# Performance work log

Hardware: AMD Instinct MI355X
Metric: run time of the kernel (lower is better)

The kernel has to match this reference:

```python
import jax, jax.numpy as jnp
import numpy as np

INPUT_SIZE = 1024
HIDDEN_SIZE = 1024
BATCH = 8192


def setup_inputs() -> dict:
    key = jax.random.key(0)
    ks = jax.random.split(key, 10)
    s_in = 1.0 / np.sqrt(INPUT_SIZE)
    s_h = 1.0 / np.sqrt(HIDDEN_SIZE)
    return {
        "input": jax.random.normal(ks[0], (BATCH, INPUT_SIZE), jnp.float32),
        "hx": jax.random.normal(ks[1], (BATCH, HIDDEN_SIZE), jnp.float32),
        # weights stored [in, out] (transpose of torch Linear)
        "W_ih": jax.random.uniform(ks[2], (INPUT_SIZE, 2 * HIDDEN_SIZE), jnp.float32, -s_in, s_in),
        "b_ih": jax.random.uniform(ks[3], (2 * HIDDEN_SIZE,), jnp.float32, -s_in, s_in),
        "W_hh": jax.random.uniform(ks[4], (HIDDEN_SIZE, 2 * HIDDEN_SIZE), jnp.float32, -s_h, s_h),
        "b_hh": jax.random.uniform(ks[5], (2 * HIDDEN_SIZE,), jnp.float32, -s_h, s_h),
        "W_c": jax.random.uniform(ks[6], (INPUT_SIZE, HIDDEN_SIZE), jnp.float32, -s_in, s_in),
        "b_c": jax.random.uniform(ks[7], (HIDDEN_SIZE,), jnp.float32, -s_in, s_in),
        "W_hc": jax.random.uniform(ks[8], (HIDDEN_SIZE, HIDDEN_SIZE), jnp.float32, -s_h, s_h),
        "b_hc": jax.random.uniform(ks[9], (HIDDEN_SIZE,), jnp.float32, -s_h, s_h),
    }


def reference(input, hx, W_ih, b_ih, W_hh, b_hh, W_c, b_c, W_hc, b_hc):
    H = hx.shape[1]
    gates = jax.nn.sigmoid(input @ W_ih + b_ih + hx @ W_hh + b_hh)  # [B, 2H]
    z_t, r_t = gates[:, :H], gates[:, H:]
    candidate = jnp.tanh(input @ W_c + b_c + r_t * (hx @ W_hc + b_hc))
    return (1.0 - z_t) * hx + z_t * candidate
```

## Files before the change

### kernel.cpp

```cpp
#include <hip/hip_runtime.h>
#include <hip/hip_bf16.h>
#include <cmath>


typedef __attribute__((ext_vector_type(8))) short bf16x8;
typedef __attribute__((ext_vector_type(4))) float f32x4;
typedef unsigned int u32;

typedef const __attribute__((address_space(1))) u32 gu32;
typedef __attribute__((address_space(3))) u32 su32;

__device__ __forceinline__ unsigned short f2bf(float f) {
  union { float f; u32 u; } v; v.f = f;
  u32 u = v.u;
  u += 0x7FFFu + ((u >> 16) & 1u);
  return (unsigned short)(u >> 16);
}
__device__ __forceinline__ float bfu(u32 w) {
  union { u32 u; float f; } c; c.u = (w & 0xffffu) << 16; return c.f;
}
__device__ __forceinline__ void gload16(void* ldsp, const void* gp) {
  __builtin_amdgcn_global_load_lds((gu32*)gp, (su32*)ldsp, 16, 0, 0);
}
__device__ __forceinline__ float sigmf(float x) { return 1.0f / (1.0f + __expf(-x)); }

__global__ __launch_bounds__(256) void cvt2(
    const float* __restrict__ In, const float* __restrict__ Hx,
    const float* __restrict__ Wih, const float* __restrict__ Whh,
    const float* __restrict__ Wc,  const float* __restrict__ Whc,
    unsigned short* __restrict__ wsIn, unsigned short* __restrict__ wsHx,
    unsigned short* __restrict__ wsW)
{
  int bid = blockIdx.x;
  if (bid < 8192) {
    int gid = bid * 256 + threadIdx.x;
    const float* src; unsigned short* dst; int idx;
    if (gid < (1 << 20)) { src = In; dst = wsIn; idx = gid; }
    else                 { src = Hx; dst = wsHx; idx = gid - (1 << 20); }
    int m = idx >> 7, u = idx & 127;
    int kt = u >> 3, s = u & 7;
    const float4* p = (const float4*)(src + (size_t)m * 1024 + kt * 64 + s * 8);
    float4 a = p[0], b = p[1];
    int row = m & 255, mt = m >> 8;
    int sp = s ^ (row & 7);
    bf16x8 v;
    v[0] = (short)f2bf(a.x); v[1] = (short)f2bf(a.y); v[2] = (short)f2bf(a.z); v[3] = (short)f2bf(a.w);
    v[4] = (short)f2bf(b.x); v[5] = (short)f2bf(b.y); v[6] = (short)f2bf(b.z); v[7] = (short)f2bf(b.w);
    *(bf16x8*)(dst + (size_t)(mt * 16 + kt) * 16384 + row * 64 + sp * 8) = v;
  } else {
    int w = bid - 8192;
    int j = w / 384, rem = w % 384;
    int t = rem >> 3, s = rem & 7;
    int jj = j & 3, f = j >> 2;
    int row = threadIdx.x;
    const float* W; int NW, k0, ncol;
    if (t < 16)      { W = Wih; NW = 2048; k0 = t * 64 + s * 8;        ncol = f * 1024 + jj * 256 + row; }
    else if (t < 32) { W = Whh; NW = 2048; k0 = (t - 16) * 64 + s * 8; ncol = f * 1024 + jj * 256 + row; }
    else             { W = f ? Whc : Wc; NW = 1024; k0 = (t - 32) * 64 + s * 8; ncol = jj * 256 + row; }
    bf16x8 v;
    #pragma unroll
    for (int b = 0; b < 8; ++b) v[b] = (short)f2bf(W[(size_t)(k0 + b) * NW + ncol]);
    int sp = s ^ (row & 7);
    *(bf16x8*)(wsW + (size_t)(j * 48 + t) * 16384 + row * 64 + sp * 8) = v;
  }
}

__global__ __launch_bounds__(512, 2) void gru_gemm1(
    const unsigned short* __restrict__ wsIn, const unsigned short* __restrict__ wsHx,
    const unsigned short* __restrict__ wsW,
    unsigned short* __restrict__ actZ, unsigned short* __restrict__ actR,
    unsigned short* __restrict__ actC, unsigned short* __restrict__ actH,
    const float* __restrict__ bih, const float* __restrict__ bhh)
{
  __shared__ unsigned short lds[65536];
  char* LB = (char*)lds;
  const int tid = threadIdx.x, lane = tid & 63, wave = tid >> 6;
  const int wm = wave >> 2, wn = wave & 3;
  const int j = blockIdx.x & 7, i = blockIdx.x >> 3;
  const int jj = j & 3, f = j >> 2;
  const int r15 = lane & 15, q = lane >> 4, x7 = r15 & 7;

  int aOff[8][2], bOff[4][2];
  #pragma unroll
  for (int mr = 0; mr < 8; ++mr)
    #pragma unroll
    for (int kk = 0; kk < 2; ++kk)
      aOff[mr][kk] = (wm * 128 + mr * 16 + r15) * 128 + (((kk * 4 + q) ^ x7) << 4);
  #pragma unroll
  for (int nr = 0; nr < 4; ++nr)
    #pragma unroll
    for (int kk = 0; kk < 2; ++kk)
      bOff[nr][kk] = 65536 + (wn * 64 + nr * 16 + r15) * 128 + (((kk * 4 + q) ^ x7) << 4);

  const unsigned short* srcW  = wsW + (size_t)j * 48 * 16384;
  const unsigned short* srcA2 = f ? wsHx : wsIn;
  const int lo8 = lane * 8;

  auto aSrc = [&](int kt) -> const unsigned short* {
    const unsigned short* base; int t;
    if (kt < 16)      { base = wsIn;  t = kt; }
    else if (kt < 32) { base = wsHx;  t = kt - 16; }
    else              { base = srcA2; t = kt - 32; }
    return base + (size_t)(i * 16 + t) * 16384;
  };
  auto stageA = [&](int PB, int kt) {
    const unsigned short* s = aSrc(kt);
    #pragma unroll
    for (int c = 0; c < 4; ++c)
      gload16(LB + PB + (wave * 4 + c) * 1024, s + (wave * 4 + c) * 512 + lo8);
  };
  auto stageB = [&](int PB, int kt) {
    const unsigned short* s = srcW + (size_t)kt * 16384;
    #pragma unroll
    for (int c = 0; c < 4; ++c)
      gload16(LB + 65536 + PB + (wave * 4 + c) * 1024, s + (wave * 4 + c) * 512 + lo8);
  };

  f32x4 acc[8][4];
  #pragma unroll
  for (int mr = 0; mr < 8; ++mr)
    #pragma unroll
    for (int nr = 0; nr < 4; ++nr) acc[mr][nr] = (f32x4)(0.0f);

  #define MG(AF, BF, MRB, NRB)                                                      \
    __builtin_amdgcn_s_setprio(1);                                                  \
    _Pragma("unroll")                                                               \
    for (int mr_ = 0; mr_ < 4; ++mr_)                                               \
      _Pragma("unroll")                                                             \
      for (int nr_ = 0; nr_ < 2; ++nr_)                                             \
        _Pragma("unroll")                                                           \
        for (int kk_ = 0; kk_ < 2; ++kk_)                                           \
          acc[(MRB)+mr_][(NRB)+nr_] = __builtin_amdgcn_mfma_f32_16x16x32_bf16(      \
              AF[mr_][kk_], BF[nr_][kk_], acc[(MRB)+mr_][(NRB)+nr_], 0, 0, 0);      \
    __builtin_amdgcn_s_setprio(0);

  #define TILE(PB, KT, KTN)                                                         \
  {                                                                                 \
    bf16x8 a0[4][2], a1[4][2], b0[2][2], b1[2][2];                                  \
    _Pragma("unroll")                                                               \
    for (int mr_ = 0; mr_ < 4; ++mr_)                                               \
      _Pragma("unroll")                                                             \
      for (int kk_ = 0; kk_ < 2; ++kk_)                                             \
        a0[mr_][kk_] = *(const bf16x8*)(LB + (PB) + aOff[mr_][kk_]);                \
    _Pragma("unroll")                                                               \
    for (int nr_ = 0; nr_ < 2; ++nr_)                                               \
      _Pragma("unroll")                                                             \
      for (int kk_ = 0; kk_ < 2; ++kk_)                                             \
        b0[nr_][kk_] = *(const bf16x8*)(LB + (PB) + bOff[nr_][kk_]);                \
    MG(a0, b0, 0, 0)                                                                \
    _Pragma("unroll")                                                               \
    for (int nr_ = 0; nr_ < 2; ++nr_)                                               \
      _Pragma("unroll")                                                             \
      for (int kk_ = 0; kk_ < 2; ++kk_)                                             \
        b1[nr_][kk_] = *(const bf16x8*)(LB + (PB) + bOff[nr_ + 2][kk_]);            \
    MG(a0, b1, 0, 2)                                                                \
    _Pragma("unroll")                                                               \
    for (int mr_ = 0; mr_ < 4; ++mr_)                                               \
      _Pragma("unroll")                                                             \
      for (int kk_ = 0; kk_ < 2; ++kk_)                                             \
        a1[mr_][kk_] = *(const bf16x8*)(LB + (PB) + aOff[mr_ + 4][kk_]);            \
    MG(a1, b0, 4, 0)                                                                \
    asm volatile("s_waitcnt lgkmcnt(0)" ::: "memory");                              \
    __builtin_amdgcn_sched_barrier(0);                                              \
    __builtin_amdgcn_s_barrier();                                                   \
    __builtin_amdgcn_sched_barrier(0);                                              \
    stageA(PB, KTN);                                                                \
    MG(a1, b1, 4, 2)                                                                \
    stageB(PB, KTN);                                                                \
    asm volatile("s_waitcnt vmcnt(8)" ::: "memory");                                \
    __builtin_amdgcn_sched_barrier(0);                                              \
    __builtin_amdgcn_s_barrier();                                                   \
    __builtin_amdgcn_sched_barrier(0);                                              \
  }

  auto dump = [&](unsigned short* dst, bool gate, float* bg) {
    #pragma unroll
    for (int mr = 0; mr < 8; ++mr)
      #pragma unroll
      for (int nr = 0; nr < 4; ++nr) {
        f32x4 t = acc[mr][nr];
        float e0, e1, e2, e3;
        if (gate) {
          e0 = sigmf(t[0] + bg[nr]); e1 = sigmf(t[1] + bg[nr]);
          e2 = sigmf(t[2] + bg[nr]); e3 = sigmf(t[3] + bg[nr]);
        } else { e0 = t[0]; e1 = t[1]; e2 = t[2]; e3 = t[3]; }
        u32 lo = (u32)f2bf(e0) | ((u32)f2bf(e1) << 16);
        u32 hi = (u32)f2bf(e2) | ((u32)f2bf(e3) << 16);
        size_t F = ((size_t)(((i * 2 + wm) * 8 + mr) * 64 + jj * 16 + wn * 4 + nr)) * 256 + lane * 4;
        uint2 uv; uv.x = lo; uv.y = hi;
        *(uint2*)(dst + F) = uv;
        acc[mr][nr] = (f32x4)(0.0f);
      }
  };

  stageA(0, 0);     stageB(0, 0);
  stageA(32768, 1); stageB(32768, 1);
  asm volatile("s_waitcnt vmcnt(0)" ::: "memory");
  __builtin_amdgcn_s_barrier();
  __builtin_amdgcn_sched_barrier(0);

  #pragma unroll 1
  for (int it = 0; it < 16; ++it) {
    int kt = 2 * it;
    TILE(0,     kt,     kt + 2)
    TILE(32768, kt + 1, kt + 3)
  }

  {
    float bg[4];
    #pragma unroll
    for (int nr = 0; nr < 4; ++nr) {
      int gn = jj * 256 + wn * 64 + nr * 16 + r15;
      int np = f ? 1024 + gn : gn;
      bg[nr] = bih[np] + bhh[np];
    }
    dump(f ? actR : actZ, true, bg);
  }

  #pragma unroll 1
  for (int it = 0; it < 8; ++it) {
    int kt = 32 + 2 * it;
    int n0 = kt + 2 <= 47 ? kt + 2 : 47;
    int n1 = kt + 3 <= 47 ? kt + 3 : 47;
    TILE(0,     kt,     n0)
    TILE(32768, kt + 1, n1)
  }

  dump(f ? actH : actC, false, nullptr);
  #undef TILE
  #undef MG
}

__global__ __launch_bounds__(256) void gru_final(
    const unsigned short* __restrict__ actZ, const unsigned short* __restrict__ actR,
    const unsigned short* __restrict__ actC, const unsigned short* __restrict__ actH,
    const float* __restrict__ Hx, const float* __restrict__ bc,
    const float* __restrict__ bhc, float* __restrict__ out)
{
  int T = blockIdx.x * 256 + threadIdx.x;
  int lane = T & 63, fr = T >> 6;
  int nr = fr & 3, wn = (fr >> 2) & 3, jj = (fr >> 4) & 3, mr = (fr >> 6) & 7, wmI = fr >> 9;
  int n  = jj * 256 + wn * 64 + nr * 16 + (lane & 15);
  int m0 = wmI * 128 + mr * 16 + ((lane >> 4) << 2);
  size_t off = (size_t)T * 4;
  uint2 zq = *(const uint2*)(actZ + off);
  uint2 rq = *(const uint2*)(actR + off);
  uint2 cq = *(const uint2*)(actC + off);
  uint2 hq = *(const uint2*)(actH + off);
  float bcv = bc[n], bhv = bhc[n];
  u32 zw[2] = { zq.x, zq.y }, rw[2] = { rq.x, rq.y };
  u32 cw[2] = { cq.x, cq.y }, hw[2] = { hq.x, hq.y };
  #pragma unroll
  for (int v = 0; v < 4; ++v) {
    int sh = (v & 1) * 16, ix = v >> 1;
    float z = bfu(zw[ix] >> sh);
    float r = bfu(rw[ix] >> sh);
    float c = bfu(cw[ix] >> sh);
    float h = bfu(hw[ix] >> sh);
    size_t adr = (size_t)(m0 + v) * 1024 + n;
    float hx = Hx[adr];
    float cand = tanhf(c + bcv + r * (h + bhv));
    out[adr] = (1.0f - z) * hx + z * cand;
  }
}

__global__ __launch_bounds__(256) void cvt_m(
    const float* __restrict__ In, const float* __restrict__ Hx,
    const float* __restrict__ Wih, const float* __restrict__ Whh,
    const float* __restrict__ Wc,  const float* __restrict__ Whc,
    unsigned short* __restrict__ wsIn, unsigned short* __restrict__ wsHx,
    unsigned short* __restrict__ wsWih, unsigned short* __restrict__ wsWhh,
    unsigned short* __restrict__ wsWc,  unsigned short* __restrict__ wsWhc)
{
  int bid = blockIdx.x;
  if (bid < 8192) {
    int gid = bid * 256 + threadIdx.x;
    const float* src; unsigned short* dst; int idx;
    if (gid < (1 << 20)) { src = In; dst = wsIn; idx = gid; }
    else                 { src = Hx; dst = wsHx; idx = gid - (1 << 20); }
    int m = idx >> 7, t = idx & 127;
    const float4* s = (const float4*)(src + (size_t)m * 1024 + t * 8);
    float4 a = s[0], b = s[1];
    int row = m & 127;
    size_t tile = (size_t)(m >> 7) * 32 + (t >> 2);
    int sw = (t & 3) ^ ((row >> 1) & 3);
    bf16x8 v;
    v[0] = (short)f2bf(a.x); v[1] = (short)f2bf(a.y); v[2] = (short)f2bf(a.z); v[3] = (short)f2bf(a.w);
    v[4] = (short)f2bf(b.x); v[5] = (short)f2bf(b.y); v[6] = (short)f2bf(b.z); v[7] = (short)f2bf(b.w);
    *(bf16x8*)(dst + tile * 4096 + row * 32 + sw * 8) = v;
  } else {
    int wb = bid - 8192;
    const float* W; unsigned short* dst; int NW; int local;
    if (wb < 1024)      { W = Wih; dst = wsWih; NW = 2048; local = wb; }
    else if (wb < 2048) { W = Whh; dst = wsWhh; NW = 2048; local = wb - 1024; }
    else if (wb < 2560) { W = Wc;  dst = wsWc;  NW = 1024; local = wb - 2048; }
    else                { W = Whc; dst = wsWhc; NW = 1024; local = wb - 2560; }
    int nb = local >> 5, kb = local & 31;
    int n  = nb * 64 + (threadIdx.x & 63);
    int k0 = kb * 32 + (threadIdx.x >> 6) * 8;
    bf16x8 v;
    #pragma unroll
    for (int b = 0; b < 8; ++b) v[b] = (short)f2bf(W[(size_t)(k0 + b) * NW + n]);
    int row = n & 63;
    size_t tile = (size_t)(n >> 6) * 32 + (k0 >> 5);
    int sw = ((k0 >> 3) & 3) ^ ((row >> 1) & 3);
    *(bf16x8*)(dst + tile * 2048 + row * 32 + sw * 8) = v;
  }
}

__global__ __launch_bounds__(256, 2) void gemm_m(
    const unsigned short* __restrict__ wsIn, const unsigned short* __restrict__ wsHx,
    const unsigned short* __restrict__ wsWih, const unsigned short* __restrict__ wsWhh,
    const unsigned short* __restrict__ wsWc, const unsigned short* __restrict__ wsWhc,
    const float* __restrict__ Hx,
    const float* __restrict__ bih, const float* __restrict__ bhh,
    const float* __restrict__ bc, const float* __restrict__ bhc,
    float* __restrict__ out)
{
  __shared__ unsigned short lds[20480];
  const int tid  = threadIdx.x;
  const int lane = tid & 63;
  const int wave = tid >> 6;
  const int wm = wave >> 1, wn = wave & 1;
  const int bid = blockIdx.x;
  const int j = bid & 15;
  const int i = bid >> 4;
  const unsigned short* srcB[10];
  int strd[10];
  #pragma unroll
  for (int c0 = 0; c0 < 10; ++c0) {
    int c = wave * 10 + c0;
    const unsigned short* p; int st;
    if (c < 8)       { p = wsIn + (size_t)i * 131072 + c * 512;        st = 4096; }
    else if (c < 16) { p = wsHx + (size_t)i * 131072 + (c - 8) * 512;  st = 4096; }
    else {
      int t = (c - 16) >> 2, cc = (c - 16) & 3;
      const unsigned short* base; int nb;
      if (t == 0)      { base = wsWih; nb = j; }
      else if (t == 1) { base = wsWih; nb = j + 16; }
      else if (t == 2) { base = wsWhh; nb = j; }
      else if (t == 3) { base = wsWhh; nb = j + 16; }
      else if (t == 4) { base = wsWc;  nb = j; }
      else             { base = wsWhc; nb = j; }
      p = base + (size_t)nb * 65536 + cc * 512;
      st = 2048;
    }
    srcB[c0] = p + lane * 8;
    strd[c0] = st;
  }
  f32x4 accZ[4][2], accR[4][2], accC[4][2], accH[4][2];
  #pragma unroll
  for (int a = 0; a < 4; ++a)
    #pragma unroll
    for (int b = 0; b < 2; ++b) {
      accZ[a][b] = (f32x4)(0.0f); accR[a][b] = (f32x4)(0.0f);
      accC[a][b] = (f32x4)(0.0f); accH[a][b] = (f32x4)(0.0f);
    }
  const int r15 = lane & 15;
  const int q   = lane >> 4;
  int aOff[4], wOff[2];
  #pragma unroll
  for (int mr = 0; mr < 4; ++mr) {
    int row = wm * 64 + mr * 16 + r15;
    aOff[mr] = row * 32 + ((q ^ ((row >> 1) & 3)) << 3);
  }
  #pragma unroll
  for (int nr = 0; nr < 2; ++nr) {
    int row = wn * 32 + nr * 16 + r15;
    wOff[nr] = row * 32 + ((q ^ ((row >> 1) & 3)) << 3);
  }
  for (int s = 0; s < 32; ++s) {
    __syncthreads();
    #pragma unroll
    for (int c0 = 0; c0 < 10; ++c0)
      gload16((void*)&lds[(wave * 10 + c0) * 512],
              (const void*)(srcB[c0] + (size_t)s * strd[c0]));
    __syncthreads();
    bf16x8 aIn[4], aHx[4];
    #pragma unroll
    for (int mr = 0; mr < 4; ++mr) {
      aIn[mr] = *(const bf16x8*)&lds[aOff[mr]];
      aHx[mr] = *(const bf16x8*)&lds[4096 + aOff[mr]];
    }
    bf16x8 wf[6][2];
    #pragma unroll
    for (int t = 0; t < 6; ++t)
      #pragma unroll
      for (int nr = 0; nr < 2; ++nr)
        wf[t][nr] = *(const bf16x8*)&lds[8192 + t * 2048 + wOff[nr]];
    #pragma unroll
    for (int mr = 0; mr < 4; ++mr)
      #pragma unroll
      for (int nr = 0; nr < 2; ++nr) {
        accZ[mr][nr] = __builtin_amdgcn_mfma_f32_16x16x32_bf16(aIn[mr], wf[0][nr], accZ[mr][nr], 0, 0, 0);
        accZ[mr][nr] = __builtin_amdgcn_mfma_f32_16x16x32_bf16(aHx[mr], wf[2][nr], accZ[mr][nr], 0, 0, 0);
        accR[mr][nr] = __builtin_amdgcn_mfma_f32_16x16x32_bf16(aIn[mr], wf[1][nr], accR[mr][nr], 0, 0, 0);
        accR[mr][nr] = __builtin_amdgcn_mfma_f32_16x16x32_bf16(aHx[mr], wf[3][nr], accR[mr][nr], 0, 0, 0);
        accC[mr][nr] = __builtin_amdgcn_mfma_f32_16x16x32_bf16(aIn[mr], wf[4][nr], accC[mr][nr], 0, 0, 0);
        accH[mr][nr] = __builtin_amdgcn_mfma_f32_16x16x32_bf16(aHx[mr], wf[5][nr], accH[mr][nr], 0, 0, 0);
      }
  }
  const int n0 = j * 64 + wn * 32;
  const int m0 = i * 128 + wm * 64;
  #pragma unroll
  for (int nr = 0; nr < 2; ++nr) {
    int n = n0 + nr * 16 + r15;
    float bz  = bih[n] + bhh[n];
    float br  = bih[1024 + n] + bhh[1024 + n];
    float bcv = bc[n], bhcv = bhc[n];
    #pragma unroll
    for (int mr = 0; mr < 4; ++mr) {
      #pragma unroll
      for (int v = 0; v < 4; ++v) {
        int m = m0 + mr * 16 + q * 4 + v;
        float z  = sigmf(accZ[mr][nr][v] + bz);
        float rr = sigmf(accR[mr][nr][v] + br);
        float cd = tanhf(accC[mr][nr][v] + bcv + rr * (accH[mr][nr][v] + bhcv));
        float h  = Hx[(size_t)m * 1024 + n];
        out[(size_t)m * 1024 + n] = (1.0f - z) * h + z * cd;
      }
    }
  }
}

__global__ __launch_bounds__(256) void gru_fallback(
    const float* __restrict__ In, const float* __restrict__ Hx,
    const float* __restrict__ Wih, const float* __restrict__ bih,
    const float* __restrict__ Whh, const float* __restrict__ bhh,
    const float* __restrict__ Wc, const float* __restrict__ bc,
    const float* __restrict__ Whc, const float* __restrict__ bhc,
    float* __restrict__ out)
{
  __shared__ float sIn[64][17], sHx[64][17];
  __shared__ float sW[6][16][68];
  const int tid = threadIdx.x;
  const int j = blockIdx.x & 15, i = blockIdx.x >> 4;
  const int tx = tid & 15, ty = tid >> 4;
  float accZ[4][4] = {}, accR[4][4] = {}, accC[4][4] = {}, accH[4][4] = {};
  const int ms = tid >> 2, kq = (tid & 3) * 4;
  const int wk = tid >> 4, wn4 = (tid & 15) * 4;
  for (int k0 = 0; k0 < 1024; k0 += 16) {
    __syncthreads();
    {
      float4 a = *(const float4*)&In[(size_t)(i * 64 + ms) * 1024 + k0 + kq];
      sIn[ms][kq] = a.x; sIn[ms][kq + 1] = a.y; sIn[ms][kq + 2] = a.z; sIn[ms][kq + 3] = a.w;
      float4 b = *(const float4*)&Hx[(size_t)(i * 64 + ms) * 1024 + k0 + kq];
      sHx[ms][kq] = b.x; sHx[ms][kq + 1] = b.y; sHx[ms][kq + 2] = b.z; sHx[ms][kq + 3] = b.w;
    }
    {
      float4 w0 = *(const float4*)&Wih[(size_t)(k0 + wk) * 2048 + j * 64 + wn4];
      float4 w1 = *(const float4*)&Wih[(size_t)(k0 + wk) * 2048 + 1024 + j * 64 + wn4];
      float4 w2 = *(const float4*)&Whh[(size_t)(k0 + wk) * 2048 + j * 64 + wn4];
      float4 w3 = *(const float4*)&Whh[(size_t)(k0 + wk) * 2048 + 1024 + j * 64 + wn4];
      float4 w4 = *(const float4*)&Wc[(size_t)(k0 + wk) * 1024 + j * 64 + wn4];
      float4 w5 = *(const float4*)&Whc[(size_t)(k0 + wk) * 1024 + j * 64 + wn4];
      sW[0][wk][wn4] = w0.x; sW[0][wk][wn4+1] = w0.y; sW[0][wk][wn4+2] = w0.z; sW[0][wk][wn4+3] = w0.w;
      sW[1][wk][wn4] = w1.x; sW[1][wk][wn4+1] = w1.y; sW[1][wk][wn4+2] = w1.z; sW[1][wk][wn4+3] = w1.w;
      sW[2][wk][wn4] = w2.x; sW[2][wk][wn4+1] = w2.y; sW[2][wk][wn4+2] = w2.z; sW[2][wk][wn4+3] = w2.w;
      sW[3][wk][wn4] = w3.x; sW[3][wk][wn4+1] = w3.y; sW[3][wk][wn4+2] = w3.z; sW[3][wk][wn4+3] = w3.w;
      sW[4][wk][wn4] = w4.x; sW[4][wk][wn4+1] = w4.y; sW[4][wk][wn4+2] = w4.z; sW[4][wk][wn4+3] = w4.w;
      sW[5][wk][wn4] = w5.x; sW[5][wk][wn4+1] = w5.y; sW[5][wk][wn4+2] = w5.z; sW[5][wk][wn4+3] = w5.w;
    }
    __syncthreads();
    for (int kk = 0; kk < 16; ++kk) {
      float aI[4], aH[4];
      #pragma unroll
      for (int im = 0; im < 4; ++im) { aI[im] = sIn[ty * 4 + im][kk]; aH[im] = sHx[ty * 4 + im][kk]; }
      #pragma unroll
      for (int jn = 0; jn < 4; ++jn) {
        float w0 = sW[0][kk][tx * 4 + jn], w1 = sW[1][kk][tx * 4 + jn], w2 = sW[2][kk][tx * 4 + jn];
        float w3 = sW[3][kk][tx * 4 + jn], w4 = sW[4][kk][tx * 4 + jn], w5 = sW[5][kk][tx * 4 + jn];
        #pragma unroll
        for (int im = 0; im < 4; ++im) {
          accZ[im][jn] += aI[im] * w0 + aH[im] * w2;
          accR[im][jn] += aI[im] * w1 + aH[im] * w3;
          accC[im][jn] += aI[im] * w4;
          accH[im][jn] += aH[im] * w5;
        }
      }
    }
  }
  #pragma unroll
  for (int jn = 0; jn < 4; ++jn) {
    int n = j * 64 + tx * 4 + jn;
    float bz  = bih[n] + bhh[n];
    float br  = bih[1024 + n] + bhh[1024 + n];
    float bcv = bc[n], bhcv = bhc[n];
    #pragma unroll
    for (int im = 0; im < 4; ++im) {
      int m = i * 64 + ty * 4 + im;
      float z  = sigmf(accZ[im][jn] + bz);
      float rr = sigmf(accR[im][jn] + br);
      float cd = tanhf(accC[im][jn] + bcv + rr * (accH[im][jn] + bhcv));
      float h  = Hx[(size_t)m * 1024 + n];
      out[(size_t)m * 1024 + n] = (1.0f - z) * h + z * cd;
    }
  }
}

extern "C" void kernel_launch(void* const* d_in, const int* in_sizes, int n_in,
                              void* d_out, int out_size, void* d_ws, size_t ws_size,
                              hipStream_t stream) {
  const float* In  = (const float*)d_in[0];
  const float* Hx  = (const float*)d_in[1];
  const float* Wih = (const float*)d_in[2];
  const float* bih = (const float*)d_in[3];
  const float* Whh = (const float*)d_in[4];
  const float* bhh = (const float*)d_in[5];
  const float* Wc  = (const float*)d_in[6];
  const float* bc  = (const float*)d_in[7];
  const float* Whc = (const float*)d_in[8];
  const float* bhc = (const float*)d_in[9];
  float* out = (float*)d_out;

  const size_t WS_BIG = 113246208ull;
  const size_t WS_MID = 46137344ull;
  if (ws_size >= WS_BIG) {
    unsigned short* ws   = (unsigned short*)d_ws;
    unsigned short* wsIn = ws;
    unsigned short* wsHx = ws + 8388608;
    unsigned short* wsW  = ws + 16777216;
    unsigned short* actZ = ws + 23068672;
    unsigned short* actR = ws + 31457280;
    unsigned short* actC = ws + 39845888;
    unsigned short* actH = ws + 48234496;
    cvt2<<<11264, 256, 0, stream>>>(In, Hx, Wih, Whh, Wc, Whc, wsIn, wsHx, wsW);
    gru_gemm1<<<256, 512, 0, stream>>>(wsIn, wsHx, wsW, actZ, actR, actC, actH, bih, bhh);
    gru_final<<<8192, 256, 0, stream>>>(actZ, actR, actC, actH, Hx, bc, bhc, out);
  } else if (ws_size >= WS_MID) {
    unsigned short* ws    = (unsigned short*)d_ws;
    unsigned short* wsIn  = ws;
    unsigned short* wsHx  = ws + 8388608;
    unsigned short* wsWih = ws + 16777216;
    unsigned short* wsWhh = ws + 18874368;
    unsigned short* wsWc  = ws + 20971520;
    unsigned short* wsWhc = ws + 22020096;
    cvt_m<<<11264, 256, 0, stream>>>(In, Hx, Wih, Whh, Wc, Whc,
                                     wsIn, wsHx, wsWih, wsWhh, wsWc, wsWhc);
    gemm_m<<<1024, 256, 0, stream>>>(wsIn, wsHx, wsWih, wsWhh, wsWc, wsWhc,
                                     Hx, bih, bhh, bc, bhc, out);
  } else {
    gru_fallback<<<2048, 256, 0, stream>>>(In, Hx, Wih, bih, Whh, bhh, Wc, bc, Whc, bhc, out);
  }
}
```

Before: 156.3 us.

## Fuse GRU epilogue into cooperative GEMM kernel with grid sync

Replaces the separate gru_final kernel with a cooperative launch: f==0 blocks dump the input-side candidate pre-activation, all blocks grid-sync, and f==1 blocks compute the final GRU output directly from their hc accumulators. This removes one kernel launch and the write and read of the actH intermediate. The TILE pipeline is also restructured with extra s_barriers interleaved between MFMA groups and LDS staging, plus a relaxed prologue wait (vmcnt(8) instead of vmcnt(0)). In exchange, the added barriers and the grid-wide sync may stall waves, and half of the blocks sit idle during the epilogue.

```diff
diff --git a/kernel.cpp b/kernel.cpp
--- a/kernel.cpp
+++ b/kernel.cpp
@@ -1,6 +1,9 @@
 #include <hip/hip_runtime.h>
 #include <hip/hip_bf16.h>
+#include <hip/hip_cooperative_groups.h>
 #include <cmath>
+
+namespace cg = cooperative_groups;
 
 
 typedef __attribute__((ext_vector_type(8))) short bf16x8;
@@ -23,6 +26,11 @@
   __builtin_amdgcn_global_load_lds((gu32*)gp, (su32*)ldsp, 16, 0, 0);
 }
 __device__ __forceinline__ float sigmf(float x) { return 1.0f / (1.0f + __expf(-x)); }
+
+#define SB0   __builtin_amdgcn_sched_barrier(0)
+#define BARR  __builtin_amdgcn_s_barrier()
+#define LGKM0 asm volatile("s_waitcnt lgkmcnt(0)" ::: "memory")
+#define VMC8  asm volatile("s_waitcnt vmcnt(8)" ::: "memory")
 
 __global__ __launch_bounds__(256) void cvt2(
     const float* __restrict__ In, const float* __restrict__ Hx,
@@ -65,15 +73,19 @@
   }
 }
 
-__global__ __launch_bounds__(512, 2) void gru_gemm1(
+__global__ __launch_bounds__(512, 2) void gru_coop(
     const unsigned short* __restrict__ wsIn, const unsigned short* __restrict__ wsHx,
     const unsigned short* __restrict__ wsW,
-    unsigned short* __restrict__ actZ, unsigned short* __restrict__ actR,
-    unsigned short* __restrict__ actC, unsigned short* __restrict__ actH,
-    const float* __restrict__ bih, const float* __restrict__ bhh)
+    unsigned short* __restrict__ actZ, unsigned short* __restrict__ actC,
+    unsigned short* __restrict__ actR,
+    const float* __restrict__ Hx,
+    const float* __restrict__ bih, const float* __restrict__ bhh,
+    const float* __restrict__ bc, const float* __restrict__ bhc,
+    float* __restrict__ out)
 {
   __shared__ unsigned short lds[65536];
   char* LB = (char*)lds;
+  cg::grid_group grid = cg::this_grid();
   const int tid = threadIdx.x, lane = tid & 63, wave = tid >> 6;
   const int wm = wave >> 2, wn = wave & 3;
   const int j = blockIdx.x & 7, i = blockIdx.x >> 3;
@@ -134,9 +146,10 @@
               AF[mr_][kk_], BF[nr_][kk_], acc[(MRB)+mr_][(NRB)+nr_], 0, 0, 0);      \
     __builtin_amdgcn_s_setprio(0);
 
-  #define TILE(PB, KT, KTN)                                                         \
+  #define TILE(PB, KTN)                                                             \
   {                                                                                 \
     bf16x8 a0[4][2], a1[4][2], b0[2][2], b1[2][2];                                  \
+                                               \
     _Pragma("unroll")                                                               \
     for (int mr_ = 0; mr_ < 4; ++mr_)                                               \
       _Pragma("unroll")                                                             \
@@ -147,30 +160,35 @@
       _Pragma("unroll")                                                             \
       for (int kk_ = 0; kk_ < 2; ++kk_)                                             \
         b0[nr_][kk_] = *(const bf16x8*)(LB + (PB) + bOff[nr_][kk_]);                \
+    BARR;                                                                           \
     MG(a0, b0, 0, 0)                                                                \
+    BARR;                                                                           \
+                                  \
     _Pragma("unroll")                                                               \
     for (int nr_ = 0; nr_ < 2; ++nr_)                                               \
       _Pragma("unroll")                                                             \
       for (int kk_ = 0; kk_ < 2; ++kk_)                                             \
         b1[nr_][kk_] = *(const bf16x8*)(LB + (PB) + bOff[nr_ + 2][kk_]);            \
-    MG(a0, b1, 0, 2)                                                                \
     _Pragma("unroll")                                                               \
     for (int mr_ = 0; mr_ < 4; ++mr_)                                               \
       _Pragma("unroll")                                                             \
       for (int kk_ = 0; kk_ < 2; ++kk_)                                             \
         a1[mr_][kk_] = *(const bf16x8*)(LB + (PB) + aOff[mr_ + 4][kk_]);            \
+    BARR;                                                                           \
+    MG(a0, b1, 0, 2)                                                                \
+    LGKM0; SB0;                                                                     \
+    BARR;                                                                           \
+                                \
+    stageA(PB, KTN);                                                                \
+    BARR;                                                                           \
     MG(a1, b0, 4, 0)                                                                \
-    asm volatile("s_waitcnt lgkmcnt(0)" ::: "memory");                              \
-    __builtin_amdgcn_sched_barrier(0);                                              \
-    __builtin_amdgcn_s_barrier();                                                   \
-    __builtin_amdgcn_sched_barrier(0);                                              \
-    stageA(PB, KTN);                                                                \
+    BARR;                                                                           \
+                               \
+    stageB(PB, KTN);                                                                \
+    VMC8; SB0;                                                                      \
+    BARR;                                                                           \
     MG(a1, b1, 4, 2)                                                                \
-    stageB(PB, KTN);                                                                \
-    asm volatile("s_waitcnt vmcnt(8)" ::: "memory");                                \
-    __builtin_amdgcn_sched_barrier(0);                                              \
-    __builtin_amdgcn_s_barrier();                                                   \
-    __builtin_amdgcn_sched_barrier(0);                                              \
+    BARR;                                                                           \
   }
 
   auto dump = [&](unsigned short* dst, bool gate, float* bg) {
@@ -195,15 +213,13 @@
 
   stageA(0, 0);     stageB(0, 0);
   stageA(32768, 1); stageB(32768, 1);
-  asm volatile("s_waitcnt vmcnt(0)" ::: "memory");
-  __builtin_amdgcn_s_barrier();
-  __builtin_amdgcn_sched_barrier(0);
+  VMC8;
+  BARR;
 
   #pragma unroll 1
-  for (int it = 0; it < 16; ++it) {
-    int kt = 2 * it;
-    TILE(0,     kt,     kt + 2)
-    TILE(32768, kt + 1, kt + 3)
+  for (int T = 0; T < 32; ++T) {
+    const int PB = (T & 1) * 32768;
+    TILE(PB, T + 2)
   }
 
   {
@@ -218,49 +234,51 @@
   }
 
   #pragma unroll 1
-  for (int it = 0; it < 8; ++it) {
-    int kt = 32 + 2 * it;
-    int n0 = kt + 2 <= 47 ? kt + 2 : 47;
-    int n1 = kt + 3 <= 47 ? kt + 3 : 47;
-    TILE(0,     kt,     n0)
-    TILE(32768, kt + 1, n1)
-  }
-
-  dump(f ? actH : actC, false, nullptr);
+  for (int T = 32; T < 48; ++T) {
+    const int PB = (T & 1) * 32768;
+    const int KTN = (T + 2 <= 47) ? T + 2 : 47;
+    TILE(PB, KTN)
+  }
   #undef TILE
   #undef MG
-}
-
-__global__ __launch_bounds__(256) void gru_final(
-    const unsigned short* __restrict__ actZ, const unsigned short* __restrict__ actR,
-    const unsigned short* __restrict__ actC, const unsigned short* __restrict__ actH,
-    const float* __restrict__ Hx, const float* __restrict__ bc,
-    const float* __restrict__ bhc, float* __restrict__ out)
-{
-  int T = blockIdx.x * 256 + threadIdx.x;
-  int lane = T & 63, fr = T >> 6;
-  int nr = fr & 3, wn = (fr >> 2) & 3, jj = (fr >> 4) & 3, mr = (fr >> 6) & 7, wmI = fr >> 9;
-  int n  = jj * 256 + wn * 64 + nr * 16 + (lane & 15);
-  int m0 = wmI * 128 + mr * 16 + ((lane >> 4) << 2);
-  size_t off = (size_t)T * 4;
-  uint2 zq = *(const uint2*)(actZ + off);
-  uint2 rq = *(const uint2*)(actR + off);
-  uint2 cq = *(const uint2*)(actC + off);
-  uint2 hq = *(const uint2*)(actH + off);
-  float bcv = bc[n], bhv = bhc[n];
-  u32 zw[2] = { zq.x, zq.y }, rw[2] = { rq.x, rq.y };
-  u32 cw[2] = { cq.x, cq.y }, hw[2] = { hq.x, hq.y };
-  #pragma unroll
-  for (int v = 0; v < 4; ++v) {
-    int sh = (v & 1) * 16, ix = v >> 1;
-    float z = bfu(zw[ix] >> sh);
-    float r = bfu(rw[ix] >> sh);
-    float c = bfu(cw[ix] >> sh);
-    float h = bfu(hw[ix] >> sh);
-    size_t adr = (size_t)(m0 + v) * 1024 + n;
-    float hx = Hx[adr];
-    float cand = tanhf(c + bcv + r * (h + bhv));
-    out[adr] = (1.0f - z) * hx + z * cand;
+
+  asm volatile("s_waitcnt vmcnt(0) lgkmcnt(0)" ::: "memory");
+
+  if (f == 0) {
+    dump(actC, false, nullptr);
+    __threadfence();
+    grid.sync();
+    return;
+  }
+
+  __threadfence();
+  grid.sync();
+
+  #pragma unroll
+  for (int nr = 0; nr < 4; ++nr) {
+    int n = jj * 256 + wn * 64 + nr * 16 + r15;
+    float bcv = bc[n], bhv = bhc[n];
+    #pragma unroll
+    for (int mr = 0; mr < 8; ++mr) {
+      size_t F = ((size_t)(((i * 2 + wm) * 8 + mr) * 64 + jj * 16 + wn * 4 + nr)) * 256 + lane * 4;
+      uint2 zq = *(const uint2*)(actZ + F);
+      uint2 cq = *(const uint2*)(actC + F);
+      uint2 rq = *(const uint2*)(actR + F);
+      u32 zw[2] = { zq.x, zq.y }, cw[2] = { cq.x, cq.y }, rw[2] = { rq.x, rq.y };
+      #pragma unroll
+      for (int v = 0; v < 4; ++v) {
+        int sh = (v & 1) * 16, ix = v >> 1;
+        float z = bfu(zw[ix] >> sh);
+        float c = bfu(cw[ix] >> sh);
+        float r = bfu(rw[ix] >> sh);
+        float hc = acc[mr][nr][v];
+        int m = i * 256 + wm * 128 + mr * 16 + q * 4 + v;
+        size_t adr = (size_t)m * 1024 + n;
+        float hx = Hx[adr];
+        float cd = tanhf(c + bcv + r * (hc + bhv));
+        out[adr] = (1.0f - z) * hx + z * cd;
+      }
+    }
   }
 }
 
@@ -513,7 +531,7 @@
   const float* bhc = (const float*)d_in[9];
   float* out = (float*)d_out;
 
-  const size_t WS_BIG = 113246208ull;
+  const size_t WS_BIG = 96468992ull;
   const size_t WS_MID = 46137344ull;
   if (ws_size >= WS_BIG) {
     unsigned short* ws   = (unsigned short*)d_ws;
@@ -521,12 +539,12 @@
     unsigned short* wsHx = ws + 8388608;
     unsigned short* wsW  = ws + 16777216;
     unsigned short* actZ = ws + 23068672;
-    unsigned short* actR = ws + 31457280;
-    unsigned short* actC = ws + 39845888;
-    unsigned short* actH = ws + 48234496;
+    unsigned short* actC = ws + 31457280;
+    unsigned short* actR = ws + 39845888;
     cvt2<<<11264, 256, 0, stream>>>(In, Hx, Wih, Whh, Wc, Whc, wsIn, wsHx, wsW);
-    gru_gemm1<<<256, 512, 0, stream>>>(wsIn, wsHx, wsW, actZ, actR, actC, actH, bih, bhh);
-    gru_final<<<8192, 256, 0, stream>>>(actZ, actR, actC, actH, Hx, bc, bhc, out);
+    void* args[] = { &wsIn, &wsHx, &wsW, &actZ, &actC, &actR,
+                     (void*)&Hx, (void*)&bih, (void*)&bhh, (void*)&bc, (void*)&bhc, &out };
+    hipLaunchCooperativeKernel((void*)gru_coop, dim3(256), dim3(512), args, 0, stream);
   } else if (ws_size >= WS_MID) {
     unsigned short* ws    = (unsigned short*)d_ws;
     unsigned short* wsIn  = ws;
```

New measurement: 289.6 us. +85.3%, slower.
